# Kernel optimization log

Measured on AMD Instinct MI355X. Metric: run time of the kernel, lower is better.

The kernel has to match this reference:

```python
import jax, jax.numpy as jnp
import numpy as np

SELECTED_CLASS = 1  # matches init_kwargs


def _edt_sq(mask):
    """Exact squared Euclidean distance of each pixel to the nearest False pixel.
    Matches scipy.ndimage.distance_transform_edt(mask)**2 (2-pass separable,
    column scan + exact row-wise parabola minimization done brute-force in chunks).
    mask: (H, W) bool.
    """
    H, W = mask.shape
    BIG = np.float32(H + W)  # > any possible true distance, safe sentinel
    g = np.where(mask, BIG, np.float32(0.0)).astype(np.float32)
    for i in range(1, H):
        np.minimum(g[i], g[i - 1] + 1, out=g[i])
    for i in range(H - 2, -1, -1):
        np.minimum(g[i], g[i + 1] + 1, out=g[i])
    g2 = g * g  # (H, W) squared column distances
    k = np.arange(W, dtype=np.float32)
    d2 = np.empty((H, W), np.float32)
    CH = 64  # chunk of output columns to bound temp memory
    for j0 in range(0, W, CH):
        j = k[j0:j0 + CH]
        diff2 = (j[None, :] - k[:, None]) ** 2  # (W, Jc)
        d2[:, j0:j0 + CH] = (g2[:, :, None] + diff2[None]).min(axis=1)
    return d2


def _inner_boundary(mask):
    """skimage.segmentation.find_boundaries(mask, mode='inner'), connectivity=1:
    foreground pixels with at least one in-image 4-neighbor in background."""
    p = np.pad(mask, 1, constant_values=True)
    ero = p[1:-1, :-2] & p[1:-1, 2:] & p[:-2, 1:-1] & p[2:, 1:-1] & mask
    return mask & ~ero


def compute_sdf_np(y_true_sel):
    """Normalized signed distance map, faithful to BoundaryLoss.compute_sdf.
    y_true_sel: (B, 1, H, W) float; returns (B, 1, H, W) float32 in [-1, 1]."""
    masks = y_true_sel[:, 0].astype(bool)
    B, H, W = masks.shape
    out = np.zeros((B, 1, H, W), np.float32)
    for b in range(B):
        m = masks[b]
        if not m.any():
            continue  # original leaves zeros
        posdis = np.sqrt(_edt_sq(m))
        negdis = np.sqrt(_edt_sq(~m))
        sdf = (negdis - negdis.min()) / (negdis.max() - negdis.min()) \
            - (posdis - posdis.min()) / (posdis.max() - posdis.min())
        sdf[_inner_boundary(m)] = 0.0
        out[b, 0] = sdf
    return out


def setup_inputs():
    key = jax.random.key(0)
    k1, k2 = jax.random.split(key)
    B, C, H, W = 8, 4, 512, 512
    y_pred = jax.random.normal(k1, (B, C, H, W), dtype=jnp.float32)
    y_true = jax.random.randint(k2, (B, C, H, W), 0, 2).astype(jnp.float32)
    return {"y_pred": y_pred, "y_true": y_true}


def reference(y_pred, y_true):
    sel = SELECTED_CLASS
    # GT signed distance map (host-side, non-differentiable, as in the original
    # which round-trips through scipy on CPU): shape (B, 1, H, W)
    gt_sdf = jnp.asarray(compute_sdf_np(np.asarray(y_true[:, sel:sel + 1])))
    pc = jax.nn.sigmoid(y_pred)  # (B, C, H, W)
    # torch.einsum('bchw,bchw->bchw', pc, dc) with dc having c=1 broadcasts over C
    mult = pc * gt_sdf
    return mult.mean(axis=(1, 2, 3)).mean()
```

## Files before the change

### kernel.cpp

```cpp
#include <hip/hip_runtime.h>
#include <math.h>

#define B 8
#define C 4
#define H 512
#define W 512
#define SEL 1
#define BIGI 1024
#define NPIX (B*H*W)
#define CH 128
#define RC 4
#define TC 32
#define NSEG 16
#define LL 8
#define CINF 3000
#define G 4

__global__ __launch_bounds__(512) void col_two_level(const float* __restrict__ ytrue,
                                                     unsigned* __restrict__ gpk,
                                                     unsigned short* __restrict__ sums) {
    __shared__ int sAp[NSEG][TC], sAn[NSEG][TC], sBp[NSEG][TC], sBn[NSEG][TC];
    int blk = blockIdx.x;
    int b   = blk >> 6;
    int rem = blk & 63;
    int jt  = rem >> 2;
    int rc  = rem & 3;
    int tx  = threadIdx.x & (TC - 1);
    int ty  = threadIdx.x / TC;
    int j   = jt * TC + tx;
    int i0  = rc * CH + ty * LL;

    const float* m = ytrue + ((size_t)b * C + SEL) * H * W + j;
    int gfp[LL], gfn[LL];
    int pp = BIGI, pn = BIGI;
    #pragma unroll
    for (int r = 0; r < LL; ++r) {
        float mv = m[(size_t)(i0 + r) * W];
        bool fg = (mv != 0.0f);
        int vp = fg ? BIGI : 0;
        int vn = fg ? 0 : BIGI;
        vp = min(vp, pp + 1); gfp[r] = vp; pp = vp;
        vn = min(vn, pn + 1); gfn[r] = vn; pn = vn;
    }
    sAp[ty][tx] = pp; sAn[ty][tx] = pn;
    __syncthreads();
    if (ty == 0) {
        int dp = BIGI, dn = BIGI;
        #pragma unroll
        for (int s = 0; s < NSEG; ++s) {
            dp = min(sAp[s][tx], dp + LL); sAp[s][tx] = dp;
            dn = min(sAn[s][tx], dn + LL); sAn[s][tx] = dn;
        }
    }
    __syncthreads();
    int cp = ty ? sAp[ty - 1][tx] : BIGI;
    int cn = ty ? sAn[ty - 1][tx] : BIGI;
    int lbp = 1 << 20, lbn = 1 << 20;
    #pragma unroll
    for (int r = 0; r < LL; ++r) {
        int vp = min(gfp[r], cp + 1 + r); gfp[r] = vp; lbp = min(lbp, vp + r);
        int vn = min(gfn[r], cn + 1 + r); gfn[r] = vn; lbn = min(lbn, vn + r);
    }
    sBp[ty][tx] = lbp; sBn[ty][tx] = lbn;
    __syncthreads();
    if (ty == 0) {
        int up = BIGI, un = BIGI;
        #pragma unroll
        for (int s = NSEG - 1; s >= 0; --s) {
            up = min(sBp[s][tx], up + LL); sBp[s][tx] = up;
            un = min(sBn[s][tx], un + LL); sBn[s][tx] = un;
        }
        unsigned short* sp = sums + (((size_t)(b * RC + rc)) * W + j) * 4;
        sp[0] = (unsigned short)sAp[NSEG - 1][tx];
        sp[1] = (unsigned short)up;
        sp[2] = (unsigned short)sAn[NSEG - 1][tx];
        sp[3] = (unsigned short)un;
    }
    __syncthreads();
    int pbp = (ty == NSEG - 1) ? BIGI : sBp[ty + 1][tx];
    int pbn = (ty == NSEG - 1) ? BIGI : sBn[ty + 1][tx];
    unsigned* op = gpk + ((size_t)b * H + i0) * W + j;
    #pragma unroll
    for (int r = LL - 1; r >= 0; --r) {
        int vp = min(gfp[r], pbp + 1); pbp = vp;
        int vn = min(gfn[r], pbn + 1); pbn = vn;
        op[(size_t)r * W] = (unsigned)vp | ((unsigned)vn << 16);
    }
}

__global__ __launch_bounds__(512) void row_fused(const unsigned* __restrict__ gpk,
                                                 const unsigned short* __restrict__ sums,
                                                 const float* __restrict__ ypred,
                                                 float* __restrict__ rowpart) {
    __shared__ float2 s2[G][W];
    __shared__ float sw[4][8];

    int blk = blockIdx.x;
    int b = blk >> 7;
    int g = blk & 127;
    int i0 = g * G;
    int rc = i0 >> 7;
    int j = threadIdx.x;

    int Ap = CINF, An = CINF, Bp = CINF, Bn = CINF;
    #pragma unroll
    for (int q = 0; q < RC; ++q) {
        if (q != rc) {
            ushort4 sv = *(const ushort4*)(sums + (((size_t)(b * RC + q)) * W + j) * 4);
            if (q < rc) {
                int e = q * CH + CH - 1;
                Ap = min(Ap, (int)sv.x - e);
                An = min(An, (int)sv.z - e);
            } else {
                int s0 = q * CH;
                Bp = min(Bp, (int)sv.y + s0);
                Bn = min(Bn, (int)sv.w + s0);
            }
        }
    }

    #pragma unroll
    for (int r = 0; r < G; ++r) {
        int ii = i0 + r;
        unsigned gv = gpk[((size_t)b * H + ii) * W + j];
        int gp = (int)(gv & 0xFFFFu), gn = (int)(gv >> 16);
        gp = min(gp, min(Ap + ii, Bp - ii));
        gn = min(gn, min(An + ii, Bn - ii));
        s2[r][j] = make_float2((float)(gp * gp), (float)(gn * gn));
    }
    __syncthreads();

    float mxp = 0.f, mxn = 0.f, A = 0.f, Bv = 0.f;
    #pragma unroll
    for (int r = 0; r < G; ++r) {
        float2 v0 = s2[r][j];
        float bp = v0.x, bn = v0.y;
        for (int rr = 1; rr < W; ++rr) {
            float r2 = (float)(rr * rr);
            if (r2 >= bp && r2 >= bn) break;
            int jl = j - rr, jr = j + rr;
            if (jl >= 0) { float2 u = s2[r][jl]; bp = fminf(bp, u.x + r2); bn = fminf(bn, u.y + r2); }
            if (jr < W)  { float2 u = s2[r][jr]; bp = fminf(bp, u.x + r2); bn = fminf(bn, u.y + r2); }
        }
        float posdis = sqrtf(bp);
        float negdis = sqrtf(bn);
        bool bnd = (bp == 1.0f);

        const float* yp = ypred + ((size_t)b * C * H + i0 + r) * W + j;
        float s = 0.f;
        #pragma unroll
        for (int cc = 0; cc < C; ++cc) {
            float x = yp[(size_t)cc * H * W];
            s += 1.0f / (1.0f + __expf(-x));
        }
        float se = bnd ? 0.f : s;
        mxp = fmaxf(mxp, bp); mxn = fmaxf(mxn, bn);
        A += se * posdis; Bv += se * negdis;
    }

    for (int off = 32; off >= 1; off >>= 1) {
        mxp = fmaxf(mxp, __shfl_down(mxp, off));
        mxn = fmaxf(mxn, __shfl_down(mxn, off));
        A  += __shfl_down(A, off);
        Bv += __shfl_down(Bv, off);
    }
    int wave = threadIdx.x >> 6, lane = threadIdx.x & 63;
    if (lane == 0) { sw[0][wave] = mxp; sw[1][wave] = mxn; sw[2][wave] = A; sw[3][wave] = Bv; }
    __syncthreads();
    if (threadIdx.x == 0) {
        float a0 = sw[0][0], a1 = sw[1][0], a2 = sw[2][0], a3 = sw[3][0];
        #pragma unroll
        for (int w = 1; w < 8; ++w) {
            a0 = fmaxf(a0, sw[0][w]); a1 = fmaxf(a1, sw[1][w]);
            a2 += sw[2][w]; a3 += sw[3][w];
        }
        *(float4*)(rowpart + (size_t)blk * 4) = make_float4(a0, a1, a2, a3);
    }
}

__global__ __launch_bounds__(512) void batch_final(const float* __restrict__ rowpart,
                                                   float* __restrict__ out) {
    __shared__ double sacc[8];
    int bw = threadIdx.x >> 6;
    int lane = threadIdx.x & 63;
    const float4* rv = (const float4*)(rowpart + (size_t)bw * 128 * 4);
    float4 e0 = rv[lane];
    float4 e1 = rv[lane + 64];
    float mxp = fmaxf(e0.x, e1.x), mxn = fmaxf(e0.y, e1.y);
    float A = e0.z + e1.z, Bv = e0.w + e1.w;
    for (int off = 32; off >= 1; off >>= 1) {
        mxp = fmaxf(mxp, __shfl_down(mxp, off));
        mxn = fmaxf(mxn, __shfl_down(mxn, off));
        A  += __shfl_down(A, off);
        Bv += __shfl_down(Bv, off);
    }
    if (lane == 0) {
        float pmax = sqrtf(mxp), nmax = sqrtf(mxn);
        float invp = (pmax > 0.f) ? 1.0f / pmax : 0.0f;
        float invn = (nmax > 0.f) ? 1.0f / nmax : 0.0f;
        sacc[bw] = (pmax > 0.f) ? (double)(invn * Bv - invp * A) : 0.0;
    }
    __syncthreads();
    if (threadIdx.x == 0) {
        double tt = 0.0;
        #pragma unroll
        for (int q = 0; q < 8; ++q) tt += sacc[q];
        out[0] = (float)(tt / (double)((size_t)B * C * H * W));
    }
}

extern "C" void kernel_launch(void* const* d_in, const int* in_sizes, int n_in,
                              void* d_out, int out_size, void* d_ws, size_t ws_size,
                              hipStream_t stream) {
    const float* ypred = (const float*)d_in[0];
    const float* ytrue = (const float*)d_in[1];
    float* out = (float*)d_out;

    unsigned* gpk = (unsigned*)d_ws;
    unsigned short* sums = (unsigned short*)(gpk + NPIX);
    float* rowpart = (float*)(sums + (size_t)B * RC * W * 4);

    col_two_level<<<512, 512, 0, stream>>>(ytrue, gpk, sums);
    row_fused<<<B * H / G, W, 0, stream>>>(gpk, sums, ypred, rowpart);
    batch_final<<<1, 512, 0, stream>>>(rowpart, out);
}
```

Baseline: 24.85 us.

## Pack column distances into 16 bits, parallel shuffle scans, finer row chunks

Column-pass output is packed into a single 16-bit value per pixel, holding the sum of positive and negative distances plus a foreground bit, instead of two 16-bit fields. This halves the intermediate traffic between the two kernels. The serial single-row segment scans in shared memory become 16-lane shuffle-based parallel prefix minimums. Row chunks shrink to 64 rows, giving 8 chunks and twice as many blocks. The trade-off is more per-column chunk summaries to combine in the row kernel and extra decode work.

```diff
diff --git a/kernel.cpp b/kernel.cpp
--- a/kernel.cpp
+++ b/kernel.cpp
@@ -8,25 +8,29 @@
 #define SEL 1
 #define BIGI 1024
 #define NPIX (B*H*W)
-#define CH 128
-#define RC 4
+#define CH 64
+#define RC 8
 #define TC 32
 #define NSEG 16
-#define LL 8
+#define LL 4
 #define CINF 3000
 #define G 4
 
 __global__ __launch_bounds__(512) void col_two_level(const float* __restrict__ ytrue,
-                                                     unsigned* __restrict__ gpk,
-                                                     unsigned short* __restrict__ sums) {
-    __shared__ int sAp[NSEG][TC], sAn[NSEG][TC], sBp[NSEG][TC], sBn[NSEG][TC];
+                                                     unsigned short* __restrict__ gpk,
+                                                     unsigned* __restrict__ sumsD,
+                                                     unsigned* __restrict__ sumsU) {
+    __shared__ int sP[NSEG][TC + 1], sN[NSEG][TC + 1];
+    __shared__ int sCP[NSEG][TC + 1], sCN[NSEG][TC + 1];
+
     int blk = blockIdx.x;
-    int b   = blk >> 6;
-    int rem = blk & 63;
-    int jt  = rem >> 2;
-    int rc  = rem & 3;
-    int tx  = threadIdx.x & (TC - 1);
-    int ty  = threadIdx.x / TC;
+    int b   = blk >> 7;
+    int rem = blk & 127;
+    int jt  = rem >> 3;
+    int rc  = rem & 7;
+    int tid = threadIdx.x;
+    int tx  = tid & (TC - 1);
+    int ty  = tid >> 5;
     int j   = jt * TC + tx;
     int i0  = rc * CH + ty * LL;
 
@@ -35,61 +39,79 @@
     int pp = BIGI, pn = BIGI;
     #pragma unroll
     for (int r = 0; r < LL; ++r) {
-        float mv = m[(size_t)(i0 + r) * W];
-        bool fg = (mv != 0.0f);
+        bool fg = (m[(size_t)(i0 + r) * W] != 0.0f);
         int vp = fg ? BIGI : 0;
         int vn = fg ? 0 : BIGI;
         vp = min(vp, pp + 1); gfp[r] = vp; pp = vp;
         vn = min(vn, pn + 1); gfn[r] = vn; pn = vn;
     }
-    sAp[ty][tx] = pp; sAn[ty][tx] = pn;
-    __syncthreads();
-    if (ty == 0) {
-        int dp = BIGI, dn = BIGI;
-        #pragma unroll
-        for (int s = 0; s < NSEG; ++s) {
-            dp = min(sAp[s][tx], dp + LL); sAp[s][tx] = dp;
-            dn = min(sAn[s][tx], dn + LL); sAn[s][tx] = dn;
-        }
-    }
-    __syncthreads();
-    int cp = ty ? sAp[ty - 1][tx] : BIGI;
-    int cn = ty ? sAn[ty - 1][tx] : BIGI;
+    sP[ty][tx] = pp - ty * LL;
+    sN[ty][tx] = pn - ty * LL;
+    __syncthreads();
+
+    int col = tid >> 4, seg = tid & 15;
+    int wp = sP[seg][col], wn = sN[seg][col];
+    #pragma unroll
+    for (int d = 1; d < NSEG; d <<= 1) {
+        int up = __shfl_up(wp, d, 16);
+        int un = __shfl_up(wn, d, 16);
+        if (seg >= d) { wp = min(wp, up); wn = min(wn, un); }
+    }
+    if (seg < NSEG - 1) {
+        sCP[seg + 1][col] = seg * LL + wp;
+        sCN[seg + 1][col] = seg * LL + wn;
+    } else {
+        int jj = jt * TC + col;
+        sumsD[((size_t)(b * RC + rc)) * W + jj] =
+            (unsigned)(seg * LL + wp) | ((unsigned)(seg * LL + wn) << 16);
+    }
+    if (seg == 0) { sCP[0][col] = BIGI; sCN[0][col] = BIGI; }
+    __syncthreads();
+
+    int cp = sCP[ty][tx], cn = sCN[ty][tx];
     int lbp = 1 << 20, lbn = 1 << 20;
     #pragma unroll
     for (int r = 0; r < LL; ++r) {
         int vp = min(gfp[r], cp + 1 + r); gfp[r] = vp; lbp = min(lbp, vp + r);
         int vn = min(gfn[r], cn + 1 + r); gfn[r] = vn; lbn = min(lbn, vn + r);
     }
-    sBp[ty][tx] = lbp; sBn[ty][tx] = lbn;
-    __syncthreads();
-    if (ty == 0) {
-        int up = BIGI, un = BIGI;
-        #pragma unroll
-        for (int s = NSEG - 1; s >= 0; --s) {
-            up = min(sBp[s][tx], up + LL); sBp[s][tx] = up;
-            un = min(sBn[s][tx], un + LL); sBn[s][tx] = un;
-        }
-        unsigned short* sp = sums + (((size_t)(b * RC + rc)) * W + j) * 4;
-        sp[0] = (unsigned short)sAp[NSEG - 1][tx];
-        sp[1] = (unsigned short)up;
-        sp[2] = (unsigned short)sAn[NSEG - 1][tx];
-        sp[3] = (unsigned short)un;
-    }
-    __syncthreads();
-    int pbp = (ty == NSEG - 1) ? BIGI : sBp[ty + 1][tx];
-    int pbn = (ty == NSEG - 1) ? BIGI : sBn[ty + 1][tx];
-    unsigned* op = gpk + ((size_t)b * H + i0) * W + j;
+    sP[ty][tx] = lbp + ty * LL;
+    sN[ty][tx] = lbn + ty * LL;
+    __syncthreads();
+
+    int w2p = sP[seg][col], w2n = sN[seg][col];
+    #pragma unroll
+    for (int d = 1; d < NSEG; d <<= 1) {
+        int up = __shfl_down(w2p, d, 16);
+        int un = __shfl_down(w2n, d, 16);
+        if (seg + d < NSEG) { w2p = min(w2p, up); w2n = min(w2n, un); }
+    }
+    if (seg > 0) {
+        sCP[seg - 1][col] = w2p - seg * LL;
+        sCN[seg - 1][col] = w2n - seg * LL;
+    } else {
+        int jj = jt * TC + col;
+        sumsU[((size_t)(b * RC + rc)) * W + jj] =
+            (unsigned)w2p | ((unsigned)w2n << 16);
+    }
+    if (seg == NSEG - 1) { sCP[NSEG - 1][col] = BIGI; sCN[NSEG - 1][col] = BIGI; }
+    __syncthreads();
+
+    int pbp = sCP[ty][tx], pbn = sCN[ty][tx];
+    unsigned short* op = gpk + ((size_t)b * H + i0) * W + j;
     #pragma unroll
     for (int r = LL - 1; r >= 0; --r) {
         int vp = min(gfp[r], pbp + 1); pbp = vp;
         int vn = min(gfn[r], pbn + 1); pbn = vn;
-        op[(size_t)r * W] = (unsigned)vp | ((unsigned)vn << 16);
-    }
-}
-
-__global__ __launch_bounds__(512) void row_fused(const unsigned* __restrict__ gpk,
-                                                 const unsigned short* __restrict__ sums,
+        int fg = (vn == 0) ? 1 : 0;
+        int g  = vp + vn;
+        op[(size_t)r * W] = (unsigned short)((g << 1) | fg);
+    }
+}
+
+__global__ __launch_bounds__(512) void row_fused(const unsigned short* __restrict__ gpk,
+                                                 const unsigned* __restrict__ sumsD,
+                                                 const unsigned* __restrict__ sumsU,
                                                  const float* __restrict__ ypred,
                                                  float* __restrict__ rowpart) {
     __shared__ float2 s2[G][W];
@@ -99,31 +121,33 @@
     int b = blk >> 7;
     int g = blk & 127;
     int i0 = g * G;
-    int rc = i0 >> 7;
+    int rc = i0 >> 6;
     int j = threadIdx.x;
 
     int Ap = CINF, An = CINF, Bp = CINF, Bn = CINF;
     #pragma unroll
     for (int q = 0; q < RC; ++q) {
-        if (q != rc) {
-            ushort4 sv = *(const ushort4*)(sums + (((size_t)(b * RC + q)) * W + j) * 4);
-            if (q < rc) {
-                int e = q * CH + CH - 1;
-                Ap = min(Ap, (int)sv.x - e);
-                An = min(An, (int)sv.z - e);
-            } else {
-                int s0 = q * CH;
-                Bp = min(Bp, (int)sv.y + s0);
-                Bn = min(Bn, (int)sv.w + s0);
-            }
+        if (q < rc) {
+            unsigned dv = sumsD[((size_t)(b * RC + q)) * W + j];
+            int e = q * CH + CH - 1;
+            Ap = min(Ap, (int)(dv & 0xFFFFu) - e);
+            An = min(An, (int)(dv >> 16) - e);
+        } else if (q > rc) {
+            unsigned uv = sumsU[((size_t)(b * RC + q)) * W + j];
+            int s0 = q * CH;
+            Bp = min(Bp, (int)(uv & 0xFFFFu) + s0);
+            Bn = min(Bn, (int)(uv >> 16) + s0);
         }
     }
 
     #pragma unroll
     for (int r = 0; r < G; ++r) {
         int ii = i0 + r;
-        unsigned gv = gpk[((size_t)b * H + ii) * W + j];
-        int gp = (int)(gv & 0xFFFFu), gn = (int)(gv >> 16);
+        unsigned v = gpk[((size_t)b * H + ii) * W + j];
+        int fg = v & 1;
+        int gv = v >> 1;
+        int gp = fg ? gv : 0;
+        int gn = fg ? 0 : gv;
         gp = min(gp, min(Ap + ii, Bp - ii));
         gn = min(gn, min(An + ii, Bn - ii));
         s2[r][j] = make_float2((float)(gp * gp), (float)(gn * gn));
@@ -216,11 +240,12 @@
     const float* ytrue = (const float*)d_in[1];
     float* out = (float*)d_out;
 
-    unsigned* gpk = (unsigned*)d_ws;
-    unsigned short* sums = (unsigned short*)(gpk + NPIX);
-    float* rowpart = (float*)(sums + (size_t)B * RC * W * 4);
-
-    col_two_level<<<512, 512, 0, stream>>>(ytrue, gpk, sums);
-    row_fused<<<B * H / G, W, 0, stream>>>(gpk, sums, ypred, rowpart);
+    unsigned short* gpk = (unsigned short*)d_ws;
+    unsigned* sumsD = (unsigned*)(gpk + NPIX);
+    unsigned* sumsU = sumsD + (size_t)B * RC * W;
+    float* rowpart = (float*)(sumsU + (size_t)B * RC * W);
+
+    col_two_level<<<B * 16 * RC, 512, 0, stream>>>(ytrue, gpk, sumsD, sumsU);
+    row_fused<<<B * H / G, W, 0, stream>>>(gpk, sumsD, sumsU, ypred, rowpart);
     batch_final<<<1, 512, 0, stream>>>(rowpart, out);
 }
```

Result: slower. 25.72 us (+3.5%).
